# Kernel tuning notes

Hardware: AMD Instinct MI355X
Metric: run time of the kernel (lower is better)

Reference implementation:

```python
import jax, jax.numpy as jnp
import numpy as np

# Model / graph dimensions
N = 10000      # number of nodes
D = 128        # feature dim (conv length axis in the original code)
K = 8          # top-k neighbors
DEG = 32       # exact out-degree used when constructing the adjacency
OUT = 128      # conv output channels
IN_CH = K + 1  # Conv1d in_channels (original code requires input_dim == k+1)


def setup_inputs() -> dict:
    key = jax.random.key(0)
    k1, k2, k3, k4 = jax.random.split(key, 4)
    node_features = jax.random.normal(k1, (N, D), jnp.float32)
    # adjacency with exactly <=DEG ones per row (duplicates collapse), so a
    # fixed-size MAX_DEG neighbor gather is exact
    nbr = jax.random.randint(k2, (N, DEG), 0, N)
    adj_matrix = jnp.zeros((N, N), jnp.int32).at[jnp.arange(N)[:, None], nbr].set(1)
    # Conv1d(in_channels=K+1, out_channels=OUT, kernel_size=K+1), torch-style init
    scale = 1.0 / np.sqrt(IN_CH * (K + 1))
    conv_w = jax.random.uniform(k3, (OUT, IN_CH, K + 1), jnp.float32, -scale, scale)
    conv_b = jax.random.uniform(k4, (OUT,), jnp.float32, -scale, scale)
    return {"node_features": node_features, "adj_matrix": adj_matrix,
            "conv_w": conv_w, "conv_b": conv_b}


def reference(node_features, adj_matrix, conv_w, conv_b):
    # --- g(): per-node neighbor gather + zero-pad-to-k + per-feature top-k ---
    # Rows have at most DEG ones, so top_k on the 0/1 row recovers all
    # neighbor indices (vals==1 marks valid slots).
    vals, idx = jax.lax.top_k(adj_matrix, DEG)                 # [N, DEG]
    gathered = node_features[idx]                               # [N, DEG, D]
    valid = (vals == 1)[..., None]                              # [N, DEG, 1]
    masked = jnp.where(valid, gathered, -jnp.inf)               # exclude non-neighbors
    # per-feature-column top-k over neighbors
    topv, _ = jax.lax.top_k(masked.transpose(0, 2, 1), K)       # [N, D, K]
    # torch pads missing neighbors with zero rows BEFORE topk; equivalently:
    # replace -inf (missing) with 0 and re-sort descending so padded zeros
    # rank above negative real values, exactly as in the original.
    topv = jnp.where(jnp.isfinite(topv), topv, 0.0)
    topv = -jnp.sort(-topv, axis=-1)                            # [N, D, K] desc
    # concat self feature row on top -> [N, K+1, D]
    sel = jnp.concatenate([node_features[:, None, :],
                           topv.transpose(0, 2, 1)], axis=1)
    # --- c(): Conv1d over the feature axis (channels = K+1, length = D) ---
    out = jax.lax.conv_general_dilated(
        sel, conv_w, window_strides=(1,), padding='VALID',
        dimension_numbers=('NCW', 'OIW', 'NCW'))                # [N, OUT, D-K]
    return out + conv_b[None, :, None]
```

## Files before the change

kernel.cpp:

```cpp
#include <hip/hip_runtime.h>
#include <cstdint>
#include <cstddef>

#define NNODES   10000
#define FD       128
#define KTOP     8
#define MAXDEG   32
#define OUT_CH   128
#define XOUT     120

typedef __attribute__((ext_vector_type(8))) short short8;
typedef __attribute__((ext_vector_type(4))) float f32x4;

#define SELT_STRIDE 24
#define SELT_ROWS   144

__device__ __forceinline__ unsigned short f2bf(float f) {
    union { float f; unsigned u; } cv; cv.f = f;
    unsigned u = cv.u;
    u += 0x7FFFu + ((u >> 16) & 1u);
    return (unsigned short)(u >> 16);
}

__global__ __launch_bounds__(256, 2)
void lgcl_fused(const float* __restrict__ nf, const int* __restrict__ adj,
                const float* __restrict__ cw, const float* __restrict__ cb,
                float* __restrict__ out)
{
    __shared__ int s_cnt;
    __shared__ int s_nbr[MAXDEG];
    __shared__ float s_g[MAXDEG * FD];
    __shared__ unsigned short s_selT[SELT_ROWS * SELT_STRIDE];

    const int tid = threadIdx.x;
    const int lane = tid & 63;
    const int wv  = tid >> 6;
    const int q   = lane >> 4;
    const int n16 = lane & 15;
    const int mh  = wv >> 1;
    const int nh  = wv & 1;

    short8 afrag[4][5];
#pragma unroll
    for (int mt = 0; mt < 4; ++mt) {
        const int o = (mh * 4 + mt) * 16 + n16;
#pragma unroll
        for (int s = 0; s < 5; ++s) {
            const int t = 2 * s + (q >> 1);
            const int c0 = (q & 1) * 8;
            short8 a;
#pragma unroll
            for (int j = 0; j < 8; ++j) {
                const int c = c0 + j;
                float v = 0.0f;
                if (c <= 8 && t <= 8) v = cw[(o * 9 + c) * 9 + t];
                a[j] = (short)f2bf(v);
            }
            afrag[mt][s] = a;
        }
    }
    f32x4 bias[4];
#pragma unroll
    for (int mt = 0; mt < 4; ++mt) {
        const int o = (mh * 4 + mt) * 16 + q * 4;
        f32x4 b;
        b[0] = cb[o]; b[1] = cb[o + 1]; b[2] = cb[o + 2]; b[3] = cb[o + 3];
        bias[mt] = b;
    }

    if (tid >= 128 && tid < 128 + (SELT_ROWS - FD)) {
        uint4* p = (uint4*)&s_selT[tid * SELT_STRIDE];
        p[0] = make_uint4(0, 0, 0, 0);
        p[1] = make_uint4(0, 0, 0, 0);
        p[2] = make_uint4(0, 0, 0, 0);
    }

    for (int node = blockIdx.x; node < NNODES; node += gridDim.x) {
        if (tid == 0) s_cnt = 0;
        __syncthreads();

        const int4* arow = (const int4*)(adj + (size_t)node * NNODES);
        for (int i = tid; i < NNODES / 4; i += 256) {
            const int4 v = arow[i];
            if (v.x == 1) { int p = atomicAdd(&s_cnt, 1); if (p < MAXDEG) s_nbr[p] = 4 * i + 0; }
            if (v.y == 1) { int p = atomicAdd(&s_cnt, 1); if (p < MAXDEG) s_nbr[p] = 4 * i + 1; }
            if (v.z == 1) { int p = atomicAdd(&s_cnt, 1); if (p < MAXDEG) s_nbr[p] = 4 * i + 2; }
            if (v.w == 1) { int p = atomicAdd(&s_cnt, 1); if (p < MAXDEG) s_nbr[p] = 4 * i + 3; }
        }
        __syncthreads();
        int m = s_cnt; if (m > MAXDEG) m = MAXDEG;

        {
            const int j = tid >> 3, l8 = tid & 7;
            if (j < m) {
                const float4* src = (const float4*)(nf + (size_t)s_nbr[j] * FD);
                float4* dst = (float4*)(s_g + j * FD);
#pragma unroll
                for (int u = 0; u < 4; ++u) dst[l8 + 8 * u] = src[l8 + 8 * u];
            }
        }
        __syncthreads();

        if (tid < FD) {
            const int d = tid;
            const float NEG = -__builtin_inff();
            float tk[8];
#pragma unroll
            for (int r = 0; r < 8; ++r) tk[r] = NEG;
            for (int j = 0; j < m; ++j) {
                float v = s_g[j * FD + d];
#pragma unroll
                for (int r = 0; r < 8; ++r) {
                    const float hi = fmaxf(tk[r], v);
                    v = fminf(tk[r], v);
                    tk[r] = hi;
                }
            }
            if (m < KTOP) {
#pragma unroll
                for (int r = 0; r < 8; ++r) tk[r] = (tk[r] == NEG) ? 0.0f : tk[r];
#pragma unroll
                for (int pass = 0; pass < 8; ++pass)
#pragma unroll
                    for (int r = 0; r < 7; ++r) {
                        const float hi = fmaxf(tk[r], tk[r + 1]);
                        const float lo = fminf(tk[r], tk[r + 1]);
                        tk[r] = hi; tk[r + 1] = lo;
                    }
            }
            const float self = nf[(size_t)node * FD + d];
            const unsigned p01 = (unsigned)f2bf(self)  | ((unsigned)f2bf(tk[0]) << 16);
            const unsigned p23 = (unsigned)f2bf(tk[1]) | ((unsigned)f2bf(tk[2]) << 16);
            const unsigned p45 = (unsigned)f2bf(tk[3]) | ((unsigned)f2bf(tk[4]) << 16);
            const unsigned p67 = (unsigned)f2bf(tk[5]) | ((unsigned)f2bf(tk[6]) << 16);
            const unsigned p8  = (unsigned)f2bf(tk[7]);
            uint4* dst = (uint4*)&s_selT[d * SELT_STRIDE];
            dst[0] = make_uint4(p01, p23, p45, p67);
            dst[1] = make_uint4(p8, 0, 0, 0);
            dst[2] = make_uint4(0, 0, 0, 0);
        }
        __syncthreads();

        f32x4 acc[4][4];
#pragma unroll
        for (int mt = 0; mt < 4; ++mt)
#pragma unroll
            for (int nt = 0; nt < 4; ++nt) acc[mt][nt] = bias[mt];

#pragma unroll
        for (int s = 0; s < 5; ++s) {
            const int t = 2 * s + (q >> 1);
            const int c0 = (q & 1) * 8;
            short8 bfrag[4];
#pragma unroll
            for (int nt = 0; nt < 4; ++nt) {
                const int n = (nh * 4 + nt) * 16 + n16;
                bfrag[nt] = *(const short8*)&s_selT[(n + t) * SELT_STRIDE + c0];
            }
#pragma unroll
            for (int mt = 0; mt < 4; ++mt)
#pragma unroll
                for (int nt = 0; nt < 4; ++nt)
                    acc[mt][nt] = __builtin_amdgcn_mfma_f32_16x16x32_bf16(
                        afrag[mt][s], bfrag[nt], acc[mt][nt], 0, 0, 0);
        }

        float* const op = out + (size_t)node * (OUT_CH * XOUT);
#pragma unroll
        for (int mt = 0; mt < 4; ++mt) {
            const int ob = (mh * 4 + mt) * 16 + q * 4;
#pragma unroll
            for (int nt = 0; nt < 4; ++nt) {
                const int x = (nh * 4 + nt) * 16 + n16;
                if (x < XOUT) {
#pragma unroll
                    for (int r = 0; r < 4; ++r)
                        op[(size_t)(ob + r) * XOUT + x] = acc[mt][nt][r];
                }
            }
        }
    }
}

extern "C" void kernel_launch(void* const* d_in, const int* in_sizes, int n_in,
                              void* d_out, int out_size, void* d_ws, size_t ws_size,
                              hipStream_t stream)
{
    (void)in_sizes; (void)n_in; (void)d_ws; (void)ws_size; (void)out_size;
    const float* nf  = (const float*)d_in[0];
    const int*   adj = (const int*)d_in[1];
    const float* cw  = (const float*)d_in[2];
    const float* cb  = (const float*)d_in[3];
    float* out = (float*)d_out;
    lgcl_fused<<<dim3(512), dim3(256), 0, stream>>>(nf, adj, cw, cb, out);
}
```

Measured before the change: 983.1 us.

## Split adjacency scan into separate kernel and software-pipeline neighbor gathers in conv

```diff
diff --git a/kernel.cpp b/kernel.cpp
--- a/kernel.cpp
+++ b/kernel.cpp
@@ -15,11 +15,251 @@
 #define SELT_STRIDE 24
 #define SELT_ROWS   144
 
+#define WS_NEEDED ((size_t)NNODES * MAXDEG * 4 + (size_t)NNODES * 4)
+
 __device__ __forceinline__ unsigned short f2bf(float f) {
     union { float f; unsigned u; } cv; cv.f = f;
     unsigned u = cv.u;
     u += 0x7FFFu + ((u >> 16) & 1u);
     return (unsigned short)(u >> 16);
+}
+
+#define BAR_LGKM() do {                                        \
+    asm volatile("s_waitcnt lgkmcnt(0)" ::: "memory");         \
+    __builtin_amdgcn_s_barrier();                              \
+    asm volatile("" ::: "memory");                             \
+} while (0)
+
+#define CHK4(v, base) do {                                                        \
+    if ((v).x == 1) { int _p = atomicAdd(&s_cnt[wv], 1); if (_p < MAXDEG) s_nbr[wv][_p] = 4 * (base) + 0; } \
+    if ((v).y == 1) { int _p = atomicAdd(&s_cnt[wv], 1); if (_p < MAXDEG) s_nbr[wv][_p] = 4 * (base) + 1; } \
+    if ((v).z == 1) { int _p = atomicAdd(&s_cnt[wv], 1); if (_p < MAXDEG) s_nbr[wv][_p] = 4 * (base) + 2; } \
+    if ((v).w == 1) { int _p = atomicAdd(&s_cnt[wv], 1); if (_p < MAXDEG) s_nbr[wv][_p] = 4 * (base) + 3; } \
+} while (0)
+
+__global__ __launch_bounds__(256, 8)
+void lgcl_scan(const int* __restrict__ adj, int* __restrict__ nbr,
+               int* __restrict__ cnt)
+{
+    __shared__ int s_nbr[4][MAXDEG];
+    __shared__ int s_cnt[4];
+    const int lane = threadIdx.x & 63;
+    const int wv   = threadIdx.x >> 6;
+    const int row  = blockIdx.x * 4 + wv;
+
+    if (lane == 0) s_cnt[wv] = 0;
+    __syncthreads();
+
+    const int4* arow = (const int4*)(adj + (size_t)row * NNODES);
+    int i = lane;
+#pragma unroll 1
+    for (int c = 0; c < 9; ++c) {
+        int4 v0 = arow[i];
+        int4 v1 = arow[i + 64];
+        int4 v2 = arow[i + 128];
+        int4 v3 = arow[i + 192];
+        CHK4(v0, i); CHK4(v1, i + 64); CHK4(v2, i + 128); CHK4(v3, i + 192);
+        i += 256;
+    }
+    {
+        int4 v0 = arow[i];
+        int4 v1 = arow[i + 64];
+        int4 v2 = arow[i + 128];
+        CHK4(v0, i); CHK4(v1, i + 64); CHK4(v2, i + 128);
+        i += 192;
+    }
+    if (i < NNODES / 4) { int4 v0 = arow[i]; CHK4(v0, i); }
+
+    __syncthreads();
+    int c = s_cnt[wv]; if (c > MAXDEG) c = MAXDEG;
+    if (lane < MAXDEG)
+        nbr[(size_t)row * MAXDEG + lane] = (lane < c) ? s_nbr[wv][lane] : 0;
+    if (lane == 0) cnt[row] = c;
+}
+
+__global__ __launch_bounds__(256, 2)
+void lgcl_conv(const float* __restrict__ nf, const int* __restrict__ nbr,
+               const int* __restrict__ cnt, const float* __restrict__ cw,
+               const float* __restrict__ cb, float* __restrict__ out)
+{
+    __shared__ float s_g[2 * MAXDEG * FD];
+    __shared__ unsigned short s_selT[SELT_ROWS * SELT_STRIDE];
+    __shared__ int s_nl[2][40];
+
+    const int tid = threadIdx.x;
+    const int lane = tid & 63;
+    const int wv  = tid >> 6;
+    const int q   = lane >> 4;
+    const int n16 = lane & 15;
+    const int mh  = wv >> 1;
+    const int nh  = wv & 1;
+    const int gj  = tid >> 3;
+    const int gl  = tid & 7;
+
+    short8 afrag[4][5];
+#pragma unroll
+    for (int mt = 0; mt < 4; ++mt) {
+        const int o = (mh * 4 + mt) * 16 + n16;
+#pragma unroll
+        for (int s = 0; s < 5; ++s) {
+            const int t = 2 * s + (q >> 1);
+            const int c0 = (q & 1) * 8;
+            short8 a;
+#pragma unroll
+            for (int j = 0; j < 8; ++j) {
+                const int c = c0 + j;
+                float v = 0.0f;
+                if (c <= 8 && t <= 8) v = cw[(o * 9 + c) * 9 + t];
+                a[j] = (short)f2bf(v);
+            }
+            afrag[mt][s] = a;
+        }
+    }
+    f32x4 bias[4];
+#pragma unroll
+    for (int mt = 0; mt < 4; ++mt) {
+        const int o = (mh * 4 + mt) * 16 + q * 4;
+        f32x4 b;
+        b[0] = cb[o]; b[1] = cb[o + 1]; b[2] = cb[o + 2]; b[3] = cb[o + 3];
+        bias[mt] = b;
+    }
+
+    if (tid >= 128 && tid < 128 + (SELT_ROWS - FD)) {
+        uint4* p = (uint4*)&s_selT[tid * SELT_STRIDE];
+        p[0] = make_uint4(0, 0, 0, 0);
+        p[1] = make_uint4(0, 0, 0, 0);
+        p[2] = make_uint4(0, 0, 0, 0);
+    }
+
+    const int G   = gridDim.x;
+    const int bid = blockIdx.x;
+    int   pb    = 0;
+    float selfv = 0.0f;
+
+    {
+        const int n0 = bid;
+        int n1 = n0 + G; if (n1 >= NNODES) n1 = n0;
+        if (tid < 33) {
+            s_nl[0][tid] = (tid < 32) ? nbr[(size_t)n0 * MAXDEG + tid] : cnt[n0];
+            s_nl[1][tid] = (tid < 32) ? nbr[(size_t)n1 * MAXDEG + tid] : cnt[n1];
+        }
+        if (tid < FD) selfv = nf[(size_t)n0 * FD + tid];
+        __syncthreads();
+        const int nidx = s_nl[0][gj];
+        const float4* gs = (const float4*)(nf + (size_t)nidx * FD);
+        float4 a0 = gs[gl], a1 = gs[gl + 8], a2 = gs[gl + 16], a3 = gs[gl + 24];
+        float4* gd = (float4*)(s_g + gj * FD);
+        gd[gl] = a0; gd[gl + 8] = a1; gd[gl + 16] = a2; gd[gl + 24] = a3;
+    }
+
+    for (int node = bid; node < NNODES; node += G) {
+        BAR_LGKM();
+
+        int n1 = node + G;     if (n1 >= NNODES) n1 = node;
+        int n2 = node + 2 * G; if (n2 >= NNODES) n2 = n1;
+
+        int nlv = 0;
+        if (tid < 33) nlv = (tid < 32) ? nbr[(size_t)n2 * MAXDEG + tid] : cnt[n2];
+
+        const int nidx = s_nl[pb ^ 1][gj];
+        const float4* gs = (const float4*)(nf + (size_t)nidx * FD);
+        float4 a0 = gs[gl], a1 = gs[gl + 8], a2 = gs[gl + 16], a3 = gs[gl + 24];
+
+        float selfnext = 0.0f;
+        if (tid < FD) selfnext = nf[(size_t)n1 * FD + tid];
+
+        const int mr = s_nl[pb][32];
+        const int m  = (mr > MAXDEG) ? MAXDEG : mr;
+
+        if (tid < FD) {
+            const int d = tid;
+            const float NEG = -__builtin_inff();
+            float tk[8];
+#pragma unroll
+            for (int r = 0; r < 8; ++r) tk[r] = NEG;
+            const float* gcol = s_g + pb * (MAXDEG * FD) + d;
+            for (int j = 0; j < m; ++j) {
+                float v = gcol[j * FD];
+#pragma unroll
+                for (int r = 0; r < 8; ++r) {
+                    const float hi = fmaxf(tk[r], v);
+                    v = fminf(tk[r], v);
+                    tk[r] = hi;
+                }
+            }
+            if (m < KTOP) {
+#pragma unroll
+                for (int r = 0; r < 8; ++r) tk[r] = (tk[r] == NEG) ? 0.0f : tk[r];
+#pragma unroll
+                for (int pass = 0; pass < 8; ++pass)
+#pragma unroll
+                    for (int r = 0; r < 7; ++r) {
+                        const float hi = fmaxf(tk[r], tk[r + 1]);
+                        const float lo = fminf(tk[r], tk[r + 1]);
+                        tk[r] = hi; tk[r + 1] = lo;
+                    }
+            }
+            const unsigned p01 = (unsigned)f2bf(selfv) | ((unsigned)f2bf(tk[0]) << 16);
+            const unsigned p23 = (unsigned)f2bf(tk[1]) | ((unsigned)f2bf(tk[2]) << 16);
+            const unsigned p45 = (unsigned)f2bf(tk[3]) | ((unsigned)f2bf(tk[4]) << 16);
+            const unsigned p67 = (unsigned)f2bf(tk[5]) | ((unsigned)f2bf(tk[6]) << 16);
+            const unsigned p8  = (unsigned)f2bf(tk[7]);
+            uint4* dst = (uint4*)&s_selT[d * SELT_STRIDE];
+            dst[0] = make_uint4(p01, p23, p45, p67);
+            dst[1] = make_uint4(p8, 0, 0, 0);
+            dst[2] = make_uint4(0, 0, 0, 0);
+        }
+
+        BAR_LGKM();
+
+        {
+            float4* gd = (float4*)(s_g + (pb ^ 1) * (MAXDEG * FD) + gj * FD);
+            gd[gl] = a0; gd[gl + 8] = a1; gd[gl + 16] = a2; gd[gl + 24] = a3;
+            if (tid < 33) s_nl[pb][tid] = nlv;
+        }
+
+        f32x4 acc[4][4];
+#pragma unroll
+        for (int mt = 0; mt < 4; ++mt)
+#pragma unroll
+            for (int nt = 0; nt < 4; ++nt) acc[mt][nt] = bias[mt];
+
+#pragma unroll
+        for (int s = 0; s < 5; ++s) {
+            const int t = 2 * s + (q >> 1);
+            const int c0 = (q & 1) * 8;
+            short8 bfrag[4];
+#pragma unroll
+            for (int nt = 0; nt < 4; ++nt) {
+                const int n = (nh * 4 + nt) * 16 + n16;
+                bfrag[nt] = *(const short8*)&s_selT[(n + t) * SELT_STRIDE + c0];
+            }
+#pragma unroll
+            for (int mt = 0; mt < 4; ++mt)
+#pragma unroll
+                for (int nt = 0; nt < 4; ++nt)
+                    acc[mt][nt] = __builtin_amdgcn_mfma_f32_16x16x32_bf16(
+                        afrag[mt][s], bfrag[nt], acc[mt][nt], 0, 0, 0);
+        }
+
+        float* const op = out + (size_t)node * (OUT_CH * XOUT);
+#pragma unroll
+        for (int mt = 0; mt < 4; ++mt) {
+            const int ob = (mh * 4 + mt) * 16 + q * 4;
+#pragma unroll
+            for (int nt = 0; nt < 4; ++nt) {
+                const int x = (nh * 4 + nt) * 16 + n16;
+                if (x < XOUT) {
+#pragma unroll
+                    for (int r = 0; r < 4; ++r)
+                        op[(size_t)(ob + r) * XOUT + x] = acc[mt][nt][r];
+                }
+            }
+        }
+
+        selfv = selfnext;
+        pb ^= 1;
+    }
 }
 
 __global__ __launch_bounds__(256, 2)
@@ -186,11 +426,19 @@
                               void* d_out, int out_size, void* d_ws, size_t ws_size,
                               hipStream_t stream)
 {
-    (void)in_sizes; (void)n_in; (void)d_ws; (void)ws_size; (void)out_size;
+    (void)in_sizes; (void)n_in; (void)out_size;
     const float* nf  = (const float*)d_in[0];
     const int*   adj = (const int*)d_in[1];
     const float* cw  = (const float*)d_in[2];
     const float* cb  = (const float*)d_in[3];
     float* out = (float*)d_out;
-    lgcl_fused<<<dim3(512), dim3(256), 0, stream>>>(nf, adj, cw, cb, out);
+
+    if (d_ws != nullptr && ws_size >= WS_NEEDED) {
+        int* nbr = (int*)d_ws;
+        int* cnt = nbr + (size_t)NNODES * MAXDEG;
+        lgcl_scan<<<dim3(2500), dim3(256), 0, stream>>>(adj, nbr, cnt);
+        lgcl_conv<<<dim3(512), dim3(256), 0, stream>>>(nf, nbr, cnt, cw, cb, out);
+    } else {
+        lgcl_fused<<<dim3(512), dim3(256), 0, stream>>>(nf, adj, cw, cb, out);
+    }
 }
```

Result: faster. 958.2 us (-2.5%).

## Split adjacency scan into separate kernel and double-buffer neighbor gathers in conv

Applied to the files above, without the earlier changes.

```diff
diff --git a/kernel.cpp b/kernel.cpp
--- a/kernel.cpp
+++ b/kernel.cpp
@@ -15,6 +15,15 @@
 #define SELT_STRIDE 24
 #define SELT_ROWS   144
 
+#define OUT_ELEMS   ((size_t)NNODES * OUT_CH * XOUT)
+#define NODE_ELEMS  (OUT_CH * XOUT)
+#define LIST_INTS   ((size_t)NNODES * 33)
+#define SCRATCH_INTS (LIST_INTS + 16)
+#define LIST_BASE   (OUT_ELEMS - SCRATCH_INTS)
+#define TAIL_FIRST  ((int)(LIST_BASE / NODE_ELEMS))
+#define NB          512
+#define LISTS_MAX   24
+
 __device__ __forceinline__ unsigned short f2bf(float f) {
     union { float f; unsigned u; } cv; cv.f = f;
     unsigned u = cv.u;
@@ -22,15 +31,68 @@
     return (unsigned short)(u >> 16);
 }
 
+#define BAR_LGKM() do {                                        \
+    asm volatile("s_waitcnt lgkmcnt(0)" ::: "memory");         \
+    __builtin_amdgcn_s_barrier();                              \
+    asm volatile("" ::: "memory");                             \
+} while (0)
+
+#define CHK4(v, base) do {                                                        \
+    if ((v).x == 1) { int _p = atomicAdd(&s_cnt[wv], 1); if (_p < MAXDEG) s_nbr[wv][_p] = 4 * (base) + 0; } \
+    if ((v).y == 1) { int _p = atomicAdd(&s_cnt[wv], 1); if (_p < MAXDEG) s_nbr[wv][_p] = 4 * (base) + 1; } \
+    if ((v).z == 1) { int _p = atomicAdd(&s_cnt[wv], 1); if (_p < MAXDEG) s_nbr[wv][_p] = 4 * (base) + 2; } \
+    if ((v).w == 1) { int _p = atomicAdd(&s_cnt[wv], 1); if (_p < MAXDEG) s_nbr[wv][_p] = 4 * (base) + 3; } \
+} while (0)
+
+__global__ __launch_bounds__(256, 8)
+void lgcl_scan(const int* __restrict__ adj, int* __restrict__ lists,
+               int* __restrict__ ctr)
+{
+    __shared__ int s_nbr[4][MAXDEG];
+    __shared__ int s_cnt[4];
+    const int lane = threadIdx.x & 63;
+    const int wv   = threadIdx.x >> 6;
+    const int row  = blockIdx.x * 4 + wv;
+
+    if (threadIdx.x == 0 && blockIdx.x == 0) atomicExch(ctr, 0);
+    if (lane == 0) s_cnt[wv] = 0;
+    __syncthreads();
+
+    const int4* arow = (const int4*)(adj + (size_t)row * NNODES);
+    int i = lane;
+#pragma unroll 1
+    for (int c = 0; c < 9; ++c) {
+        int4 v0 = arow[i];
+        int4 v1 = arow[i + 64];
+        int4 v2 = arow[i + 128];
+        int4 v3 = arow[i + 192];
+        CHK4(v0, i); CHK4(v1, i + 64); CHK4(v2, i + 128); CHK4(v3, i + 192);
+        i += 256;
+    }
+    {
+        int4 v0 = arow[i];
+        int4 v1 = arow[i + 64];
+        int4 v2 = arow[i + 128];
+        CHK4(v0, i); CHK4(v1, i + 64); CHK4(v2, i + 128);
+        i += 192;
+    }
+    if (i < NNODES / 4) { int4 v0 = arow[i]; CHK4(v0, i); }
+
+    __syncthreads();
+    int c = s_cnt[wv]; if (c > MAXDEG) c = MAXDEG;
+    if (lane < MAXDEG)
+        lists[(size_t)row * 33 + lane] = (lane < c) ? s_nbr[wv][lane] : 0;
+    if (lane == 0) lists[(size_t)row * 33 + 32] = c;
+}
+
 __global__ __launch_bounds__(256, 2)
-void lgcl_fused(const float* __restrict__ nf, const int* __restrict__ adj,
-                const float* __restrict__ cw, const float* __restrict__ cb,
-                float* __restrict__ out)
+void lgcl_conv(const float* __restrict__ nf, const int* __restrict__ lists,
+               int* __restrict__ ctr, const float* __restrict__ cw,
+               const float* __restrict__ cb, float* __restrict__ out)
 {
-    __shared__ int s_cnt;
-    __shared__ int s_nbr[MAXDEG];
-    __shared__ float s_g[MAXDEG * FD];
+    __shared__ float s_g[2 * MAXDEG * FD];
     __shared__ unsigned short s_selT[SELT_ROWS * SELT_STRIDE];
+    __shared__ int s_lists[LISTS_MAX * 33];
 
     const int tid = threadIdx.x;
     const int lane = tid & 63;
@@ -39,6 +101,21 @@
     const int n16 = lane & 15;
     const int mh  = wv >> 1;
     const int nh  = wv & 1;
+    const int gj  = tid >> 3;
+    const int gl  = tid & 7;
+
+    const int bid = blockIdx.x;
+    const bool tail = (bid == NB - 1);
+    const int nbase  = tail ? TAIL_FIRST : bid;
+    const int stride = tail ? 1 : (NB - 1);
+    const int mycnt  = tail ? (NNODES - TAIL_FIRST)
+                            : ((TAIL_FIRST - 1 - bid) / (NB - 1) + 1);
+
+    for (int idx = tid; idx < mycnt * 33; idx += 256) {
+        const int i = idx / 33;
+        const int j = idx - 33 * i;
+        s_lists[idx] = lists[(size_t)(nbase + i * stride) * 33 + j];
+    }
 
     short8 afrag[4][5];
 #pragma unroll
@@ -75,31 +152,39 @@
         p[2] = make_uint4(0, 0, 0, 0);
     }
 
-    for (int node = blockIdx.x; node < NNODES; node += gridDim.x) {
-        if (tid == 0) s_cnt = 0;
-        __syncthreads();
-
-        const int4* arow = (const int4*)(adj + (size_t)node * NNODES);
-        for (int i = tid; i < NNODES / 4; i += 256) {
-            const int4 v = arow[i];
-            if (v.x == 1) { int p = atomicAdd(&s_cnt, 1); if (p < MAXDEG) s_nbr[p] = 4 * i + 0; }
-            if (v.y == 1) { int p = atomicAdd(&s_cnt, 1); if (p < MAXDEG) s_nbr[p] = 4 * i + 1; }
-            if (v.z == 1) { int p = atomicAdd(&s_cnt, 1); if (p < MAXDEG) s_nbr[p] = 4 * i + 2; }
-            if (v.w == 1) { int p = atomicAdd(&s_cnt, 1); if (p < MAXDEG) s_nbr[p] = 4 * i + 3; }
-        }
-        __syncthreads();
-        int m = s_cnt; if (m > MAXDEG) m = MAXDEG;
-
-        {
-            const int j = tid >> 3, l8 = tid & 7;
-            if (j < m) {
-                const float4* src = (const float4*)(nf + (size_t)s_nbr[j] * FD);
-                float4* dst = (float4*)(s_g + j * FD);
-#pragma unroll
-                for (int u = 0; u < 4; ++u) dst[l8 + 8 * u] = src[l8 + 8 * u];
-            }
-        }
-        __syncthreads();
+    __syncthreads();
+    if (tid == 0) {
+        __threadfence();
+        atomicAdd(ctr, 1);
+        if (tail) { while (atomicAdd(ctr, 0) < NB) { } }
+    }
+    __syncthreads();
+
+    int   pb    = 0;
+    float selfv = 0.0f;
+    {
+        const int nidx = s_lists[gj];
+        const float4* gs = (const float4*)(nf + (size_t)nidx * FD);
+        float4 a0 = gs[gl], a1 = gs[gl + 8], a2 = gs[gl + 16], a3 = gs[gl + 24];
+        float4* gd = (float4*)(s_g + gj * FD);
+        gd[gl] = a0; gd[gl + 8] = a1; gd[gl + 16] = a2; gd[gl + 24] = a3;
+        if (tid < FD) selfv = nf[(size_t)nbase * FD + tid];
+    }
+
+    for (int it = 0; it < mycnt; ++it) {
+        const int node = nbase + it * stride;
+        BAR_LGKM();
+
+        const int itn  = (it + 1 < mycnt) ? it + 1 : it;
+        const int nidx = s_lists[itn * 33 + gj];
+        const float4* gs = (const float4*)(nf + (size_t)nidx * FD);
+        float4 a0 = gs[gl], a1 = gs[gl + 8], a2 = gs[gl + 16], a3 = gs[gl + 24];
+
+        float selfnext = 0.0f;
+        if (tid < FD) selfnext = nf[(size_t)(nbase + itn * stride) * FD + tid];
+
+        const int mr = s_lists[it * 33 + 32];
+        const int m  = (mr > MAXDEG) ? MAXDEG : mr;
 
         if (tid < FD) {
             const int d = tid;
@@ -107,8 +192,9 @@
             float tk[8];
 #pragma unroll
             for (int r = 0; r < 8; ++r) tk[r] = NEG;
+            const float* gcol = s_g + pb * (MAXDEG * FD) + d;
             for (int j = 0; j < m; ++j) {
-                float v = s_g[j * FD + d];
+                float v = gcol[j * FD];
 #pragma unroll
                 for (int r = 0; r < 8; ++r) {
                     const float hi = fmaxf(tk[r], v);
@@ -128,8 +214,7 @@
                         tk[r] = hi; tk[r + 1] = lo;
                     }
             }
-            const float self = nf[(size_t)node * FD + d];
-            const unsigned p01 = (unsigned)f2bf(self)  | ((unsigned)f2bf(tk[0]) << 16);
+            const unsigned p01 = (unsigned)f2bf(selfv) | ((unsigned)f2bf(tk[0]) << 16);
             const unsigned p23 = (unsigned)f2bf(tk[1]) | ((unsigned)f2bf(tk[2]) << 16);
             const unsigned p45 = (unsigned)f2bf(tk[3]) | ((unsigned)f2bf(tk[4]) << 16);
             const unsigned p67 = (unsigned)f2bf(tk[5]) | ((unsigned)f2bf(tk[6]) << 16);
@@ -139,7 +224,13 @@
             dst[1] = make_uint4(p8, 0, 0, 0);
             dst[2] = make_uint4(0, 0, 0, 0);
         }
-        __syncthreads();
+
+        BAR_LGKM();
+
+        {
+            float4* gd = (float4*)(s_g + (pb ^ 1) * (MAXDEG * FD) + gj * FD);
+            gd[gl] = a0; gd[gl + 8] = a1; gd[gl + 16] = a2; gd[gl + 24] = a3;
+        }
 
         f32x4 acc[4][4];
 #pragma unroll
@@ -179,6 +270,9 @@
                 }
             }
         }
+
+        selfv = selfnext;
+        pb ^= 1;
     }
 }
 
@@ -186,11 +280,16 @@
                               void* d_out, int out_size, void* d_ws, size_t ws_size,
                               hipStream_t stream)
 {
-    (void)in_sizes; (void)n_in; (void)d_ws; (void)ws_size; (void)out_size;
+    (void)in_sizes; (void)n_in; (void)out_size; (void)d_ws; (void)ws_size;
     const float* nf  = (const float*)d_in[0];
     const int*   adj = (const int*)d_in[1];
     const float* cw  = (const float*)d_in[2];
     const float* cb  = (const float*)d_in[3];
     float* out = (float*)d_out;
-    lgcl_fused<<<dim3(512), dim3(256), 0, stream>>>(nf, adj, cw, cb, out);
-}
+
+    int* lists = (int*)(out + LIST_BASE);
+    int* ctr   = lists + LIST_INTS;
+
+    lgcl_scan<<<dim3(2500), dim3(256), 0, stream>>>(adj, lists, ctr);
+    lgcl_conv<<<dim3(NB), dim3(256), 0, stream>>>(nf, lists, ctr, cw, cb, out);
+}
```

After: 969.0 us. Within noise of the previous version (-1.4%).
